# Optimization experiments

Measured on AMD Instinct MI355X. Metric: run time of the kernel, lower is better.

The kernel has to match this reference:

```python
import jax, jax.numpy as jnp
import numpy as np

N_NODES = 100000
N_EDGES = 1600000
IN_FEATS = 128
N_HIDDEN = 128
N_CLASSES = 47


def _glorot(key, shape):
    fan_in, fan_out = shape
    lim = jnp.sqrt(6.0 / (fan_in + fan_out))
    return jax.random.uniform(key, shape, jnp.float32, -lim, lim)


def setup_inputs() -> dict:
    key = jax.random.key(0)
    ks = jax.random.split(key, 12)
    x = jax.random.normal(ks[0], (N_NODES, IN_FEATS), jnp.float32)
    src = jax.random.randint(ks[1], (N_EDGES,), 0, N_NODES, jnp.int32)
    dst = jax.random.randint(ks[2], (N_EDGES,), 0, N_NODES, jnp.int32)
    dims = [(IN_FEATS, N_HIDDEN), (N_HIDDEN, N_HIDDEN), (N_HIDDEN, N_CLASSES)]
    params = {}
    for l, (di, do) in enumerate(dims):
        params[f"Ws{l}"] = _glorot(ks[3 + 3 * l], (di, do))
        params[f"Wn{l}"] = _glorot(ks[4 + 3 * l], (di, do))
        params[f"b{l}"] = jnp.zeros((do,), jnp.float32)
    return {"x": x, "src": src, "dst": dst, **params}


def _sage_layer(h, src, dst, Ws, Wn, b):
    # mean aggregation over incoming edges (irregular gather + segment-reduce)
    n = h.shape[0]
    msg = h[src]  # [E, F]
    agg = jax.ops.segment_sum(msg, dst, num_segments=n)
    deg = jax.ops.segment_sum(jnp.ones((src.shape[0],), h.dtype), dst, num_segments=n)
    agg = agg / jnp.maximum(deg, 1.0)[:, None]
    return h @ Ws + agg @ Wn + b


def reference(x, src, dst, Ws0, Wn0, b0, Ws1, Wn1, b1, Ws2, Wn2, b2):
    layers = [(Ws0, Wn0, b0), (Ws1, Wn1, b1), (Ws2, Wn2, b2)]
    h = x
    for l, (Ws, Wn, b) in enumerate(layers):
        h = _sage_layer(h, src, dst, Ws, Wn, b)
        if l != len(layers) - 1:
            h = jax.nn.relu(h)  # dropout is identity at inference
    return h
```

## Files before the change

kernel.cpp:

```cpp
#include <hip/hip_runtime.h>
#include <cstdint>
#include <cstddef>

static const int NN = 100000;
static const int NE = 1600000;
static const int F  = 128;
static const int BKT_SHIFT = 9;
static const int BNODES = 1 << BKT_SHIFT;
static const int NBKT = (NN + BNODES - 1) >> BKT_SHIFT;
static const int PKCAP = 16384;
static const int SRC_BITS = 17;
static const unsigned SRC_MASK = (1u << SRC_BITS) - 1u;

typedef __attribute__((ext_vector_type(8))) short short8;
typedef __attribute__((ext_vector_type(4))) float float4v;
typedef __attribute__((ext_vector_type(2))) float f32x2;

static __device__ __forceinline__ unsigned f2bf(float f){
    unsigned u = __builtin_bit_cast(unsigned, f);
    return (u + 0x7FFFu + ((u >> 16) & 1u)) >> 16;
}
static __device__ __forceinline__ float bf_lo(unsigned u){
    return __builtin_bit_cast(float, u << 16);
}
static __device__ __forceinline__ float bf_hi(unsigned u){
    return __builtin_bit_cast(float, u & 0xFFFF0000u);
}

__global__ __launch_bounds__(256) void bscatter_k(
        const int* __restrict__ src, const int* __restrict__ dst,
        int* __restrict__ bfill, unsigned* __restrict__ pk, int E){
    __shared__ int hist[NBKT];
    __shared__ int gbase[NBKT];
    const int t = threadIdx.x;
    for (int i = t; i < NBKT; i += 256) hist[i] = 0;
    __syncthreads();
    const int e0 = blockIdx.x * 2048;
    int s[8], d[8], b[8], r[8];
    #pragma unroll
    for (int j = 0; j < 8; ++j){
        int e = e0 + j*256 + t;
        if (e < E){
            s[j] = src[e]; d[j] = dst[e];
            b[j] = d[j] >> BKT_SHIFT;
            r[j] = atomicAdd(&hist[b[j]], 1);
        }
    }
    __syncthreads();
    for (int i = t; i < NBKT; i += 256){
        int h = hist[i];
        int base = 0;
        if (h) base = atomicAdd(&bfill[i], h);
        gbase[i] = i*PKCAP + base;
    }
    __syncthreads();
    #pragma unroll
    for (int j = 0; j < 8; ++j){
        int e = e0 + j*256 + t;
        if (e < E)
            pk[gbase[b[j]] + r[j]] =
                (unsigned)s[j] | ((unsigned)(d[j] & (BNODES-1)) << SRC_BITS);
    }
}

__global__ __launch_bounds__(1024) void sort_k(
        const unsigned* __restrict__ pk, const int* __restrict__ bfill,
        int* __restrict__ row_ptr, int* __restrict__ ssorted, int N){
    __shared__ int bs[256];
    __shared__ int hc[BNODES];
    __shared__ int of[BNODES];
    __shared__ int fi[BNODES];
    const int b = blockIdx.x;
    const int t = threadIdx.x;
    if (t < 256) bs[t] = (t < NBKT) ? bfill[t] : 0;
    if (t < BNODES){ hc[t] = 0; fi[t] = 0; }
    __syncthreads();
    for (int off = 1; off < 256; off <<= 1){
        int add = (t < 256 && t >= off) ? bs[t-off] : 0;
        __syncthreads();
        if (t < 256) bs[t] += add;
        __syncthreads();
    }
    const int cntb = bfill[b];
    const int rbeg = bs[b] - cntb;
    const unsigned* mypk = pk + (size_t)b * PKCAP;
    for (int i = t; i < cntb; i += 1024)
        atomicAdd(&hc[mypk[i] >> SRC_BITS], 1);
    __syncthreads();
    if (t < BNODES) of[t] = hc[t];
    __syncthreads();
    for (int off = 1; off < BNODES; off <<= 1){
        int add = (t < BNODES && t >= off) ? of[t-off] : 0;
        __syncthreads();
        if (t < BNODES) of[t] += add;
        __syncthreads();
    }
    if (t < BNODES){
        int excl = of[t] - hc[t];
        of[t] = excl;
        int node = (b << BKT_SHIFT) + t;
        if (node < N) row_ptr[node] = rbeg + excl;
    }
    if (b == 0 && t == 0) row_ptr[N] = NE;
    __syncthreads();
    for (int i = t; i < cntb; i += 1024){
        unsigned p = mypk[i];
        int dl = (int)(p >> SRC_BITS);
        int pos = rbeg + of[dl] + atomicAdd(&fi[dl], 1);
        ssorted[pos] = (int)(p & SRC_MASK);
    }
}


__global__ void xconv_k(const float* __restrict__ x, unsigned short* __restrict__ xb, int n8){
    int i = blockIdx.x*256 + threadIdx.x;
    if (i < n8){
        float4 v0 = ((const float4*)x)[i*2];
        float4 v1 = ((const float4*)x)[i*2+1];
        uint4 o;
        o.x = f2bf(v0.x) | (f2bf(v0.y) << 16);
        o.y = f2bf(v0.z) | (f2bf(v0.w) << 16);
        o.z = f2bf(v1.x) | (f2bf(v1.y) << 16);
        o.w = f2bf(v1.z) | (f2bf(v1.w) << 16);
        ((uint4*)xb)[i] = o;
    }
}

__global__ void prepw_all_k(const float* __restrict__ Ws0, const float* __restrict__ Wn0,
                            const float* __restrict__ Ws1, const float* __restrict__ Wn1,
                            const float* __restrict__ Ws2, const float* __restrict__ Wn2,
                            unsigned short* __restrict__ Wt0, unsigned short* __restrict__ Wt1,
                            unsigned short* __restrict__ Wt2){
    int i = blockIdx.x*256 + threadIdx.x;
    const float* Ws; const float* Wn; unsigned short* Wt; int D; int idx;
    if (i < 32768){       Ws=Ws0; Wn=Wn0; Wt=Wt0; D=128; idx=i; }
    else if (i < 65536){  Ws=Ws1; Wn=Wn1; Wt=Wt1; D=128; idx=i-32768; }
    else {                Ws=Ws2; Wn=Wn2; Wt=Wt2; D=47;  idx=i-65536; }
    int n = idx >> 7, k = idx & 127;
    float v = 0.f;
    if (n < D)        v = Ws[k*D + n];
    else if (n < 2*D) v = Wn[k*D + (n - D)];
    Wt[n*128 + k] = (unsigned short)f2bf(v);
}


__global__ __launch_bounds__(256) void gemm_mfma_k(
        const unsigned short* __restrict__ hb,
        const unsigned short* __restrict__ Wt,
        const float* __restrict__ bias,
        unsigned short* __restrict__ Y,
        unsigned short* __restrict__ Z,
        int M, int D, int Dpad){
    __shared__ char ldsA[128*256];
    const int t = threadIdx.x;
    const int lane = t & 63;
    const int w = t >> 6;
    const int wm = w >> 1, wn = w & 1;
    const int tile = blockIdx.x * 128;
    const int cbase = blockIdx.y * 128;

    #pragma unroll
    for (int i = 0; i < 8; ++i){
        int chunkid = i*4 + w;
        int lin = chunkid*64 + lane;
        int row = lin >> 4;
        int cs  = lin & 15;
        int grow = tile + row; if (grow >= M) grow = M - 1;
        const char* src = (const char*)hb + (size_t)grow*256 + ((size_t)(cs ^ (row & 7)) << 4);
        __builtin_amdgcn_global_load_lds(
            (const __attribute__((address_space(1))) void*)src,
            (__attribute__((address_space(3))) void*)(ldsA + (size_t)chunkid*1024 + (size_t)lane*16),
            16, 0, 0);
    }

    short8 bfrag[4][4];
    {
        int ncol = cbase + wn*64;
        #pragma unroll
        for (int n = 0; n < 4; ++n){
            int wrow = ncol + n*16 + (lane & 15);
            const unsigned short* bp = Wt + (size_t)wrow*128 + ((lane >> 4) * 8);
            #pragma unroll
            for (int kk = 0; kk < 4; ++kk)
                bfrag[n][kk] = *(const short8*)(bp + kk*32);
        }
    }

    float4v acc[4][4];
    #pragma unroll
    for (int m = 0; m < 4; ++m)
        #pragma unroll
        for (int n = 0; n < 4; ++n)
            acc[m][n] = (float4v){0.f,0.f,0.f,0.f};

    __syncthreads();

    #pragma unroll
    for (int m = 0; m < 4; ++m){
        int r = wm*64 + m*16 + (lane & 15);
        #pragma unroll
        for (int kk = 0; kk < 4; ++kk){
            int c = kk*4 + (lane >> 4);
            short8 a = *(const short8*)(ldsA + (size_t)r*256 + ((size_t)(c ^ (r & 7)) << 4));
            #pragma unroll
            for (int n = 0; n < 4; ++n)
                acc[m][n] = __builtin_amdgcn_mfma_f32_16x16x32_bf16(a, bfrag[n][kk], acc[m][n], 0, 0, 0);
        }
    }

    #pragma unroll
    for (int m = 0; m < 4; ++m){
        #pragma unroll
        for (int n = 0; n < 4; ++n){
            int c = cbase + wn*64 + n*16 + (lane & 15);
            #pragma unroll
            for (int j = 0; j < 4; ++j){
                int r = tile + wm*64 + m*16 + (lane >> 4)*4 + j;
                if (r < M){
                    float v = acc[m][n][j];
                    if (c < D){
                        v += bias[c];
                        Y[(size_t)r*Dpad + c] = (unsigned short)f2bf(v);
                    } else if (c < 2*D){
                        Z[(size_t)r*Dpad + (c - D)] = (unsigned short)f2bf(v);
                    }
                }
            }
        }
    }
}


__global__ __launch_bounds__(256) void agg128_k(
        const unsigned short* __restrict__ Yb, const unsigned short* __restrict__ Zb,
        const int* __restrict__ row_ptr, const int* __restrict__ ssorted,
        unsigned short* __restrict__ hout, int N){
    const int lane = threadIdx.x & 63;
    const int q   = lane >> 4;
    const int sub = lane & 15;
    const int node = blockIdx.x*4 + (threadIdx.x >> 6);
    if (node >= N) return;
    const int beg = __builtin_amdgcn_readfirstlane(row_ptr[node]);
    const int end = __builtin_amdgcn_readfirstlane(row_ptr[node+1]);
    const float inv = 1.0f / fmaxf((float)(end - beg), 1.0f);
    const char* zc = (const char*)Zb;
    const unsigned boff = (unsigned)(sub*16);
    f32x2 a0={0.f,0.f}, a1={0.f,0.f}, a2={0.f,0.f}, a3={0.f,0.f};
    for (int e = beg; e < end; e += 32){
        int s[8];
        #pragma unroll
        for (int j = 0; j < 8; ++j){
            int ei = e + 4*j + q;
            int ec = ei < end ? ei : end - 1;
            s[j] = ssorted[ec];
        }
        uint4 u[8];
        #pragma unroll
        for (int j = 0; j < 8; ++j){
            int ei = e + 4*j + q;
            if (ei < end)
                u[j] = *(const uint4*)(zc + ((unsigned)s[j]*256u + boff));
        }
        #pragma unroll
        for (int j = 0; j < 8; ++j){
            if (e + 4*j + q < end){
                a0 += (f32x2){ bf_lo(u[j].x), bf_hi(u[j].x) };
                a1 += (f32x2){ bf_lo(u[j].y), bf_hi(u[j].y) };
                a2 += (f32x2){ bf_lo(u[j].z), bf_hi(u[j].z) };
                a3 += (f32x2){ bf_lo(u[j].w), bf_hi(u[j].w) };
            }
        }
    }
    a0.x += __shfl_xor(a0.x,16,64); a0.x += __shfl_xor(a0.x,32,64);
    a0.y += __shfl_xor(a0.y,16,64); a0.y += __shfl_xor(a0.y,32,64);
    a1.x += __shfl_xor(a1.x,16,64); a1.x += __shfl_xor(a1.x,32,64);
    a1.y += __shfl_xor(a1.y,16,64); a1.y += __shfl_xor(a1.y,32,64);
    a2.x += __shfl_xor(a2.x,16,64); a2.x += __shfl_xor(a2.x,32,64);
    a2.y += __shfl_xor(a2.y,16,64); a2.y += __shfl_xor(a2.y,32,64);
    a3.x += __shfl_xor(a3.x,16,64); a3.x += __shfl_xor(a3.x,32,64);
    a3.y += __shfl_xor(a3.y,16,64); a3.y += __shfl_xor(a3.y,32,64);
    if (q == 0){
        uint4 yu = *(const uint4*)((const char*)Yb + (size_t)node*256 + sub*16);
        float r0 = fmaxf(bf_lo(yu.x) + a0.x*inv, 0.f);
        float r1 = fmaxf(bf_hi(yu.x) + a0.y*inv, 0.f);
        float r2 = fmaxf(bf_lo(yu.y) + a1.x*inv, 0.f);
        float r3 = fmaxf(bf_hi(yu.y) + a1.y*inv, 0.f);
        float r4 = fmaxf(bf_lo(yu.z) + a2.x*inv, 0.f);
        float r5 = fmaxf(bf_hi(yu.z) + a2.y*inv, 0.f);
        float r6 = fmaxf(bf_lo(yu.w) + a3.x*inv, 0.f);
        float r7 = fmaxf(bf_hi(yu.w) + a3.y*inv, 0.f);
        uint4 o;
        o.x = f2bf(r0) | (f2bf(r1) << 16);
        o.y = f2bf(r2) | (f2bf(r3) << 16);
        o.z = f2bf(r4) | (f2bf(r5) << 16);
        o.w = f2bf(r6) | (f2bf(r7) << 16);
        *(uint4*)((char*)hout + (size_t)node*256 + sub*16) = o;
    }
}

__global__ __launch_bounds__(256) void aggfin_k(
        const unsigned short* __restrict__ Yb, const unsigned short* __restrict__ Zb,
        const int* __restrict__ row_ptr, const int* __restrict__ ssorted,
        float* __restrict__ out, int N){
    const int lane = threadIdx.x & 63;
    const int q   = lane >> 4;
    const int sub = lane & 15;
    const int node = blockIdx.x*4 + (threadIdx.x >> 6);
    if (node >= N) return;
    const int beg = __builtin_amdgcn_readfirstlane(row_ptr[node]);
    const int end = __builtin_amdgcn_readfirstlane(row_ptr[node+1]);
    const float inv = 1.0f / fmaxf((float)(end - beg), 1.0f);
    const char* zc = (const char*)Zb;
    const bool act = (sub < 12);
    const unsigned boff = (unsigned)(sub*8);
    f32x2 acc0 = {0.f,0.f}, acc1 = {0.f,0.f};
    for (int e = beg; e < end; e += 32){
        int s[8];
        #pragma unroll
        for (int j = 0; j < 8; ++j){
            int ei = e + 4*j + q;
            int ec = ei < end ? ei : end - 1;
            s[j] = ssorted[ec];
        }
        uint2 u[8];
        #pragma unroll
        for (int j = 0; j < 8; ++j){
            int ei = e + 4*j + q;
            if (act && ei < end)
                u[j] = *(const uint2*)(zc + ((unsigned)s[j]*96u + boff));
        }
        #pragma unroll
        for (int j = 0; j < 8; ++j){
            if (act && e + 4*j + q < end){
                acc0 += (f32x2){ bf_lo(u[j].x), bf_lo(u[j].y) };
                acc1 += (f32x2){ bf_hi(u[j].x), bf_hi(u[j].y) };
            }
        }
    }
    acc0.x += __shfl_xor(acc0.x, 16, 64); acc0.x += __shfl_xor(acc0.x, 32, 64);
    acc0.y += __shfl_xor(acc0.y, 16, 64); acc0.y += __shfl_xor(acc0.y, 32, 64);
    acc1.x += __shfl_xor(acc1.x, 16, 64); acc1.x += __shfl_xor(acc1.x, 32, 64);
    acc1.y += __shfl_xor(acc1.y, 16, 64); acc1.y += __shfl_xor(acc1.y, 32, 64);
    if (q == 0 && act){
        uint2 yu = *(const uint2*)((const char*)Yb + (size_t)node*96 + sub*8);
        float r0 = bf_lo(yu.x) + acc0.x*inv;
        float r1 = bf_hi(yu.x) + acc1.x*inv;
        float r2 = bf_lo(yu.y) + acc0.y*inv;
        float r3 = bf_hi(yu.y) + acc1.y*inv;
        int f = 4*sub;
        size_t o = (size_t)node*47 + f;
        out[o]   = r0;
        out[o+1] = r1;
        out[o+2] = r2;
        if (f + 3 < 47) out[o+3] = r3;
    }
}


extern "C" void kernel_launch(void* const* d_in, const int* in_sizes, int n_in,
                              void* d_out, int out_size, void* d_ws, size_t ws_size,
                              hipStream_t stream){
    const float* x   = (const float*)d_in[0];
    const int*   src = (const int*)  d_in[1];
    const int*   dstv= (const int*)  d_in[2];
    const float* Ws0 = (const float*)d_in[3];
    const float* Wn0 = (const float*)d_in[4];
    const float* b0  = (const float*)d_in[5];
    const float* Ws1 = (const float*)d_in[6];
    const float* Wn1 = (const float*)d_in[7];
    const float* b1  = (const float*)d_in[8];
    const float* Ws2 = (const float*)d_in[9];
    const float* Wn2 = (const float*)d_in[10];
    const float* b2  = (const float*)d_in[11];
    float* out = (float*)d_out;
    const int N = NN, E = NE;

    char* w = (char*)d_ws;
    size_t off = 0;
    auto alloc = [&](size_t bytes)->char*{
        char* p = w + off; off += (bytes + 255) & ~(size_t)255; return p;
    };
    int*   bfill   = (int*)  alloc((size_t)NBKT*4);
    int*   row_ptr = (int*)  alloc((size_t)(NN+1)*4);
    int*   ssorted = (int*)  alloc((size_t)E*4);
    unsigned* pk   = (unsigned*)alloc((size_t)NBKT*PKCAP*4);
    unsigned short* xb  = (unsigned short*)alloc((size_t)NN*F*2);
    unsigned short* hA  = (unsigned short*)alloc((size_t)NN*F*2);
    unsigned short* hB  = (unsigned short*)alloc((size_t)NN*F*2);
    unsigned short* Yb  = (unsigned short*)alloc((size_t)NN*F*2);
    unsigned short* Zb  = (unsigned short*)alloc((size_t)NN*F*2);
    unsigned short* Wt0 = (unsigned short*)alloc((size_t)256*128*2);
    unsigned short* Wt1 = (unsigned short*)alloc((size_t)256*128*2);
    unsigned short* Wt2 = (unsigned short*)alloc((size_t)128*128*2);
    (void)ws_size; (void)n_in; (void)in_sizes; (void)out_size;

    const int GE = (E + 2047)/2048;

    hipMemsetAsync(bfill, 0, (size_t)NBKT*4, stream);
    bscatter_k<<<GE, 256, 0, stream>>>(src, dstv, bfill, pk, E);
    sort_k    <<<NBKT, 1024, 0, stream>>>(pk, bfill, row_ptr, ssorted, N);

    xconv_k<<<(N*F/8 + 255)/256, 256, 0, stream>>>(x, xb, N*F/8);
    prepw_all_k<<<320, 256, 0, stream>>>(Ws0, Wn0, Ws1, Wn1, Ws2, Wn2, Wt0, Wt1, Wt2);

    const int GM = (N + 127)/128;
    const int GA = (N + 3)/4;

    gemm_mfma_k<<<dim3(GM,2), 256, 0, stream>>>(xb, Wt0, b0, Yb, Zb, N, 128, 128);
    agg128_k   <<<GA, 256, 0, stream>>>(Yb, Zb, row_ptr, ssorted, hA, N);
    gemm_mfma_k<<<dim3(GM,2), 256, 0, stream>>>(hA, Wt1, b1, Yb, Zb, N, 128, 128);
    agg128_k   <<<GA, 256, 0, stream>>>(Yb, Zb, row_ptr, ssorted, hB, N);
    gemm_mfma_k<<<dim3(GM,1), 256, 0, stream>>>(hB, Wt2, b2, Yb, Zb, N, 47, 48);
    aggfin_k   <<<GA, 256, 0, stream>>>(Yb, Zb, row_ptr, ssorted, out, N);
}
```

Measured before the change: 359.1 us.

## Remap GEMM block order, drop gather predication, widen final-layer rows to 128B

The GEMM grid becomes 1D with an interleaved block mapping, so the two column halves of the same row tiles run close together and share the A tile in L2. The agg128 gather loads become unconditional, since clamped indices are always valid. The final layer pads Dpad from 48 to 64, so Y/Z rows are 128 bytes and aggfin gathers full 16-byte chunks with 8 edge slots per wave instead of 8-byte chunks with idle lanes. This adds redundant loads on tail edges and larger Y/Z writes for layer 3, and depends on the not-shown GEMM epilogue handling Dpad=64 correctly.

New measurement: 366.8 us. 1.02x slower.

```diff
diff --git a/kernel.cpp b/kernel.cpp
--- a/kernel.cpp
+++ b/kernel.cpp
@@ -150,14 +150,21 @@
         const float* __restrict__ bias,
         unsigned short* __restrict__ Y,
         unsigned short* __restrict__ Z,
-        int M, int D, int Dpad){
+        int M, int D, int Dpad, int two_pass){
     __shared__ char ldsA[128*256];
     const int t = threadIdx.x;
     const int lane = t & 63;
     const int w = t >> 6;
     const int wm = w >> 1, wn = w & 1;
-    const int tile = blockIdx.x * 128;
-    const int cbase = blockIdx.y * 128;
+    int bid = blockIdx.x;
+    int bx, by;
+    if (two_pass){
+        bx = (bid >> 4)*8 + (bid & 7);
+        by = (bid >> 3) & 1;
+    } else { bx = bid; by = 0; }
+    const int tile = bx * 128;
+    if (tile >= M) return;
+    const int cbase = by * 128;
 
     #pragma unroll
     for (int i = 0; i < 8; ++i){
@@ -256,11 +263,8 @@
         }
         uint4 u[8];
         #pragma unroll
-        for (int j = 0; j < 8; ++j){
-            int ei = e + 4*j + q;
-            if (ei < end)
-                u[j] = *(const uint4*)(zc + ((unsigned)s[j]*256u + boff));
-        }
+        for (int j = 0; j < 8; ++j)
+            u[j] = *(const uint4*)(zc + ((unsigned)s[j]*256u + boff));
         #pragma unroll
         for (int j = 0; j < 8; ++j){
             if (e + 4*j + q < end){
@@ -303,56 +307,62 @@
         const int* __restrict__ row_ptr, const int* __restrict__ ssorted,
         float* __restrict__ out, int N){
     const int lane = threadIdx.x & 63;
-    const int q   = lane >> 4;
-    const int sub = lane & 15;
+    const int slot = lane >> 3;
+    const int sub  = lane & 7;
     const int node = blockIdx.x*4 + (threadIdx.x >> 6);
     if (node >= N) return;
     const int beg = __builtin_amdgcn_readfirstlane(row_ptr[node]);
     const int end = __builtin_amdgcn_readfirstlane(row_ptr[node+1]);
     const float inv = 1.0f / fmaxf((float)(end - beg), 1.0f);
     const char* zc = (const char*)Zb;
-    const bool act = (sub < 12);
-    const unsigned boff = (unsigned)(sub*8);
-    f32x2 acc0 = {0.f,0.f}, acc1 = {0.f,0.f};
+    const unsigned boff = (unsigned)(sub*16);
+    f32x2 a0={0.f,0.f}, a1={0.f,0.f}, a2={0.f,0.f}, a3={0.f,0.f};
     for (int e = beg; e < end; e += 32){
-        int s[8];
-        #pragma unroll
-        for (int j = 0; j < 8; ++j){
-            int ei = e + 4*j + q;
+        int s[4];
+        #pragma unroll
+        for (int j = 0; j < 4; ++j){
+            int ei = e + 8*j + slot;
             int ec = ei < end ? ei : end - 1;
             s[j] = ssorted[ec];
         }
-        uint2 u[8];
-        #pragma unroll
-        for (int j = 0; j < 8; ++j){
-            int ei = e + 4*j + q;
-            if (act && ei < end)
-                u[j] = *(const uint2*)(zc + ((unsigned)s[j]*96u + boff));
-        }
-        #pragma unroll
-        for (int j = 0; j < 8; ++j){
-            if (act && e + 4*j + q < end){
-                acc0 += (f32x2){ bf_lo(u[j].x), bf_lo(u[j].y) };
-                acc1 += (f32x2){ bf_hi(u[j].x), bf_hi(u[j].y) };
+        uint4 u[4];
+        #pragma unroll
+        for (int j = 0; j < 4; ++j)
+            u[j] = *(const uint4*)(zc + ((unsigned)s[j]*128u + boff));
+        #pragma unroll
+        for (int j = 0; j < 4; ++j){
+            if (e + 8*j + slot < end){
+                a0 += (f32x2){ bf_lo(u[j].x), bf_hi(u[j].x) };
+                a1 += (f32x2){ bf_lo(u[j].y), bf_hi(u[j].y) };
+                a2 += (f32x2){ bf_lo(u[j].z), bf_hi(u[j].z) };
+                a3 += (f32x2){ bf_lo(u[j].w), bf_hi(u[j].w) };
             }
         }
     }
-    acc0.x += __shfl_xor(acc0.x, 16, 64); acc0.x += __shfl_xor(acc0.x, 32, 64);
-    acc0.y += __shfl_xor(acc0.y, 16, 64); acc0.y += __shfl_xor(acc0.y, 32, 64);
-    acc1.x += __shfl_xor(acc1.x, 16, 64); acc1.x += __shfl_xor(acc1.x, 32, 64);
-    acc1.y += __shfl_xor(acc1.y, 16, 64); acc1.y += __shfl_xor(acc1.y, 32, 64);
-    if (q == 0 && act){
-        uint2 yu = *(const uint2*)((const char*)Yb + (size_t)node*96 + sub*8);
-        float r0 = bf_lo(yu.x) + acc0.x*inv;
-        float r1 = bf_hi(yu.x) + acc1.x*inv;
-        float r2 = bf_lo(yu.y) + acc0.y*inv;
-        float r3 = bf_hi(yu.y) + acc1.y*inv;
-        int f = 4*sub;
+    a0.x += __shfl_xor(a0.x,8,64); a0.x += __shfl_xor(a0.x,16,64); a0.x += __shfl_xor(a0.x,32,64);
+    a0.y += __shfl_xor(a0.y,8,64); a0.y += __shfl_xor(a0.y,16,64); a0.y += __shfl_xor(a0.y,32,64);
+    a1.x += __shfl_xor(a1.x,8,64); a1.x += __shfl_xor(a1.x,16,64); a1.x += __shfl_xor(a1.x,32,64);
+    a1.y += __shfl_xor(a1.y,8,64); a1.y += __shfl_xor(a1.y,16,64); a1.y += __shfl_xor(a1.y,32,64);
+    a2.x += __shfl_xor(a2.x,8,64); a2.x += __shfl_xor(a2.x,16,64); a2.x += __shfl_xor(a2.x,32,64);
+    a2.y += __shfl_xor(a2.y,8,64); a2.y += __shfl_xor(a2.y,16,64); a2.y += __shfl_xor(a2.y,32,64);
+    a3.x += __shfl_xor(a3.x,8,64); a3.x += __shfl_xor(a3.x,16,64); a3.x += __shfl_xor(a3.x,32,64);
+    a3.y += __shfl_xor(a3.y,8,64); a3.y += __shfl_xor(a3.y,16,64); a3.y += __shfl_xor(a3.y,32,64);
+    if (slot == 0){
+        uint4 yu = *(const uint4*)((const char*)Yb + (size_t)node*128 + sub*16);
+        float v[8];
+        v[0] = bf_lo(yu.x) + a0.x*inv;
+        v[1] = bf_hi(yu.x) + a0.y*inv;
+        v[2] = bf_lo(yu.y) + a1.x*inv;
+        v[3] = bf_hi(yu.y) + a1.y*inv;
+        v[4] = bf_lo(yu.z) + a2.x*inv;
+        v[5] = bf_hi(yu.z) + a2.y*inv;
+        v[6] = bf_lo(yu.w) + a3.x*inv;
+        v[7] = bf_hi(yu.w) + a3.y*inv;
+        int f = sub*8;
         size_t o = (size_t)node*47 + f;
-        out[o]   = r0;
-        out[o+1] = r1;
-        out[o+2] = r2;
-        if (f + 3 < 47) out[o+3] = r3;
+        #pragma unroll
+        for (int k = 0; k < 8; ++k)
+            if (f + k < 47) out[o + k] = v[k];
     }
 }
 
@@ -404,12 +414,13 @@
     prepw_all_k<<<320, 256, 0, stream>>>(Ws0, Wn0, Ws1, Wn1, Ws2, Wn2, Wt0, Wt1, Wt2);
 
     const int GM = (N + 127)/128;
+    const int G2 = ((GM + 7)/8) * 16;
     const int GA = (N + 3)/4;
 
-    gemm_mfma_k<<<dim3(GM,2), 256, 0, stream>>>(xb, Wt0, b0, Yb, Zb, N, 128, 128);
+    gemm_mfma_k<<<G2, 256, 0, stream>>>(xb, Wt0, b0, Yb, Zb, N, 128, 128, 1);
     agg128_k   <<<GA, 256, 0, stream>>>(Yb, Zb, row_ptr, ssorted, hA, N);
-    gemm_mfma_k<<<dim3(GM,2), 256, 0, stream>>>(hA, Wt1, b1, Yb, Zb, N, 128, 128);
+    gemm_mfma_k<<<G2, 256, 0, stream>>>(hA, Wt1, b1, Yb, Zb, N, 128, 128, 1);
     agg128_k   <<<GA, 256, 0, stream>>>(Yb, Zb, row_ptr, ssorted, hB, N);
-    gemm_mfma_k<<<dim3(GM,1), 256, 0, stream>>>(hB, Wt2, b2, Yb, Zb, N, 47, 48);
+    gemm_mfma_k<<<GM, 256, 0, stream>>>(hB, Wt2, b2, Yb, Zb, N, 47, 64, 0);
     aggfin_k   <<<GA, 256, 0, stream>>>(Yb, Zb, row_ptr, ssorted, out, N);
 }
```
